# Performance work log

Measured on AMD Instinct MI355X. Metric: run time of the kernel, lower is better.

## Reference

```python
import jax, jax.numpy as jnp
import numpy as np

N = 50000
E = 800000
NODE_DIM = 15
HID = 64
HEADS = 4
NEG_SLOPE = 0.2


def _add_self_loops(edge_index, n):
    loops = jnp.arange(n, dtype=edge_index.dtype)
    src = jnp.concatenate([edge_index[0], loops])
    dst = jnp.concatenate([edge_index[1], loops])
    return src, dst


def gat_conv(x, edge_index, W, att_src, att_dst, bias, concat):
    # x: [N, F_in]; W: [F_in, heads*out]; att_*: [heads, out]; bias: [heads*out] or [out]
    n = x.shape[0]
    heads, out_dim = att_src.shape
    src, dst = _add_self_loops(edge_index, n)
    h = (x @ W).reshape(n, heads, out_dim)              # [N, H, D]
    a_src = jnp.sum(h * att_src[None], axis=-1)          # [N, H]
    a_dst = jnp.sum(h * att_dst[None], axis=-1)          # [N, H]
    e = a_src[src] + a_dst[dst]                          # [E', H]
    e = jnp.where(e > 0, e, NEG_SLOPE * e)               # LeakyReLU(0.2)
    # segment softmax over incoming edges of each dst node
    m = jax.ops.segment_max(e, dst, num_segments=n)      # [N, H]
    m = jnp.where(jnp.isfinite(m), m, 0.0)
    w = jnp.exp(e - m[dst])                              # [E', H]
    z = jax.ops.segment_sum(w, dst, num_segments=n)      # [N, H]
    alpha = w / z[dst]                                   # [E', H]
    msg = alpha[:, :, None] * h[src]                     # [E', H, D]
    out = jax.ops.segment_sum(msg, dst, num_segments=n)  # [N, H, D]
    if concat:
        return out.reshape(n, heads * out_dim) + bias
    return out.mean(axis=1) + bias


def setup_inputs() -> dict:
    key = jax.random.key(0)
    ks = jax.random.split(key, 11)
    x = jax.random.normal(ks[0], (N, NODE_DIM), dtype=jnp.float32)
    edge_index = jax.random.randint(ks[1], (2, E), 0, N, dtype=jnp.int64)
    s1 = 1.0 / np.sqrt(NODE_DIM)
    s2 = 1.0 / np.sqrt(HEADS * HID)
    return {
        "x": x,
        "edge_index": edge_index,
        "W1": jax.random.normal(ks[2], (NODE_DIM, HEADS * HID), dtype=jnp.float32) * s1,
        "att_src1": jax.random.normal(ks[3], (HEADS, HID), dtype=jnp.float32) * s2,
        "att_dst1": jax.random.normal(ks[4], (HEADS, HID), dtype=jnp.float32) * s2,
        "b1": jnp.zeros((HEADS * HID,), dtype=jnp.float32),
        "W2": jax.random.normal(ks[5], (HEADS * HID, HID), dtype=jnp.float32) * s2,
        "att_src2": jax.random.normal(ks[6], (1, HID), dtype=jnp.float32) * s2,
        "att_dst2": jax.random.normal(ks[7], (1, HID), dtype=jnp.float32) * s2,
        "b2": jnp.zeros((HID,), dtype=jnp.float32),
    }


def reference(x, edge_index, W1, att_src1, att_dst1, b1, W2, att_src2, att_dst2, b2):
    h = gat_conv(x, edge_index, W1, att_src1, att_dst1, b1, concat=True)   # [N, 256]
    h = jax.nn.elu(h)
    # dropout p=0.2 skipped (eval mode)
    h = gat_conv(h, edge_index, W2, att_src2, att_dst2, b2, concat=True)   # heads=1 -> [N, 64]
    return h.mean(axis=0)                                                   # [64]
```

## Files before the change

### kernel.cpp

```cpp
#include <hip/hip_runtime.h>
#include <hip/hip_fp16.h>

#define NNODES 50000
#define NEDGES 800000
#define NEG_SLOPE 0.2f
#define NTOT (NEDGES + NNODES)
#define NB_NODE ((NNODES + 255) / 256)
#define CHUNK 4096
#define NCHUNK ((NEDGES + CHUNK - 1) / CHUNK)
#define CAPB 4800
#define CNTSTRIDE 16

typedef _Float16 half8 __attribute__((ext_vector_type(8)));
typedef _Float16 half4 __attribute__((ext_vector_type(4)));
typedef float f32x4 __attribute__((ext_vector_type(4)));

__global__ void setup_kernel(const float* __restrict__ x, const float* __restrict__ W1,
                             const float* __restrict__ att_src, const float* __restrict__ att_dst,
                             const float* __restrict__ W2,
                             int* __restrict__ bucket_cnt, float* __restrict__ x16,
                             float* __restrict__ asrc4, float* __restrict__ adst4,
                             _Float16* __restrict__ W2T) {
    int b = blockIdx.x, t = threadIdx.x;
    __shared__ float swa[16][4], swd[16][4];
    if (t < 128) {
        int k = (t & 63) >> 2, h = t & 3;
        float s = 0.f;
        if (k < 15) {
            const float* att = (t < 64) ? att_src : att_dst;
#pragma unroll 16
            for (int d = 0; d < 64; ++d)
                s += W1[k * 256 + h * 64 + d] * att[h * 64 + d];
        }
        if (t < 64) swa[k][h] = s; else swd[k][h] = s;
    }
    int tid = b * 256 + t;
    if (tid < NB_NODE * CNTSTRIDE) bucket_cnt[tid] = 0;
    if (tid < 64 * 256) {
        int n = tid >> 8, k = tid & 255;
        W2T[n * 256 + k] = (_Float16)W2[k * 64 + n];
    }
    __syncthreads();
    int nid = tid;
    if (nid < NNODES) {
        float xv[16];
#pragma unroll
        for (int k = 0; k < 15; ++k) xv[k] = x[nid * 15 + k];
        xv[15] = 0.f;
#pragma unroll
        for (int k = 0; k < 16; k += 4)
            *(float4*)(x16 + (size_t)nid * 16 + k) = make_float4(xv[k], xv[k+1], xv[k+2], xv[k+3]);
        float ps[4] = {0.f, 0.f, 0.f, 0.f}, pd[4] = {0.f, 0.f, 0.f, 0.f};
#pragma unroll
        for (int k = 0; k < 15; ++k)
#pragma unroll
            for (int h = 0; h < 4; ++h) {
                ps[h] += xv[k] * swa[k][h];
                pd[h] += xv[k] * swd[k][h];
            }
        *(float4*)(asrc4 + nid * 4) = make_float4(ps[0], ps[1], ps[2], ps[3]);
        *(float4*)(adst4 + nid * 4) = make_float4(pd[0], pd[1], pd[2], pd[3]);
    }
}

__global__ void bucket_scatter(const int* __restrict__ srcs, const int* __restrict__ dsts,
                               int* __restrict__ bucket_cnt, int* __restrict__ bucketbuf) {
    int b = blockIdx.x, t = threadIdx.x;
    __shared__ unsigned short meta[CHUNK];
    __shared__ int lcnt[NB_NODE], lbase[NB_NODE];
    for (int i = t; i < NB_NODE; i += 256) lcnt[i] = 0;
    __syncthreads();
    int e0 = b * CHUNK;
    int e1 = e0 + CHUNK; if (e1 > NEDGES) e1 = NEDGES;
    for (int e = e0 + t; e < e1; e += 256) {
        int d = dsts[e];
        meta[e - e0] = (unsigned short)d;
        atomicAdd(&lcnt[d >> 8], 1);
    }
    __syncthreads();
    for (int i = t; i < NB_NODE; i += 256) {
        int c = lcnt[i];
        lbase[i] = c ? atomicAdd(&bucket_cnt[i * CNTSTRIDE], c) : 0;
    }
    __syncthreads();
    for (int i = t; i < NB_NODE; i += 256) lcnt[i] = 0;
    __syncthreads();
    for (int e = e0 + t; e < e1; e += 256) {
        int dv = meta[e - e0];
        int bk = dv >> 8;
        int pos = lbase[bk] + atomicAdd(&lcnt[bk], 1);
        if (pos < CAPB) bucketbuf[bk * CAPB + pos] = ((dv & 255) << 16) | srcs[e];
    }
}

__global__ void scanA(const int* __restrict__ bucket_cnt, const int* __restrict__ bucketbuf,
                      int* __restrict__ rowstart, int* __restrict__ partials) {
    int b = blockIdx.x, t = threadIdx.x, lane = t & 63, wid = t >> 6;
    __shared__ int hist[256];
    __shared__ int ws[4];
    int i = b * 256 + t;
    hist[t] = (i < NNODES) ? 1 : 0;
    __syncthreads();
    int n = bucket_cnt[b * CNTSTRIDE]; if (n > CAPB) n = CAPB;
    const int* buf = bucketbuf + (size_t)b * CAPB;
    for (int j = t; j < n; j += 256)
        atomicAdd(&hist[buf[j] >> 16], 1);
    __syncthreads();
    int v = (i < NNODES) ? hist[t] : 0;
    int incl = v;
#pragma unroll
    for (int off = 1; off < 64; off <<= 1) {
        int u = __shfl_up(incl, off, 64);
        if (lane >= off) incl += u;
    }
    if (lane == 63) ws[wid] = incl;
    __syncthreads();
    int w0 = ws[0], w1 = ws[1], w2 = ws[2], w3 = ws[3];
    int woff = (wid > 0 ? w0 : 0) + (wid > 1 ? w1 : 0) + (wid > 2 ? w2 : 0);
    if (i < NNODES) rowstart[i] = woff + (incl - v);
    if (t == 0) partials[b] = w0 + w1 + w2 + w3;
}

__global__ void scanB(const int* __restrict__ partials, int* __restrict__ blockoff,
                      int* __restrict__ rowstart, int nb) {
    int t = threadIdx.x, lane = t & 63, wid = t >> 6;
    int v = (t < nb) ? partials[t] : 0;
    int incl = v;
#pragma unroll
    for (int off = 1; off < 64; off <<= 1) {
        int u = __shfl_up(incl, off, 64);
        if (lane >= off) incl += u;
    }
    __shared__ int ws[4];
    if (lane == 63) ws[wid] = incl;
    __syncthreads();
    int w0 = ws[0], w1 = ws[1], w2 = ws[2], w3 = ws[3];
    int woff = (wid > 0 ? w0 : 0) + (wid > 1 ? w1 : 0) + (wid > 2 ? w2 : 0);
    if (t < nb) blockoff[t] = woff + (incl - v);
    if (t == 0) rowstart[NNODES] = w0 + w1 + w2 + w3;
}

__global__ void scanC(int* __restrict__ rowstart, const int* __restrict__ blockoff) {
    int b = blockIdx.x, t = threadIdx.x;
    int i = b * 256 + t;
    if (i < NNODES) rowstart[i] += blockoff[b];
}

__global__ void local_sort(const int* __restrict__ bucket_cnt, const int* __restrict__ bucketbuf,
                           const int* __restrict__ rowstart, int* __restrict__ srclist) {
    int b = blockIdx.x, t = threadIdx.x;
    __shared__ int cur[256];
    __shared__ int local[8192];
    int idx = b * 256 + t; if (idx > NNODES) idx = NNODES;
    int base = rowstart[b * 256];
    cur[t] = rowstart[idx] - base;
    __syncthreads();
    int nid = b * 256 + t;
    if (nid < NNODES) {
        int pos = atomicAdd(&cur[t], 1);
        local[pos] = nid;
    }
    int n = bucket_cnt[b * CNTSTRIDE]; if (n > CAPB) n = CAPB;
    const int* buf = bucketbuf + (size_t)b * CAPB;
    for (int i = t; i < n; i += 256) {
        int entry = buf[i];
        int pos = atomicAdd(&cur[entry >> 16], 1);
        local[pos] = entry & 0xFFFF;
    }
    __syncthreads();
    int endidx = (b + 1) * 256; if (endidx > NNODES) endidx = NNODES;
    int total = rowstart[endidx] - base;
    for (int i = t; i < total; i += 256) srclist[base + i] = local[i];
}

__global__ void layer1_aggr(const float* __restrict__ x16, const int* __restrict__ rowstart,
                            const int* __restrict__ srclist,
                            const float* __restrict__ asrc4, const float* __restrict__ adst4,
                            const float* __restrict__ W1, const float* __restrict__ b1,
                            __half* __restrict__ out1) {
    int wid = threadIdx.x >> 6, lane = threadIdx.x & 63;
    int nid = blockIdx.x * 4 + wid;
    int h = lane >> 4, k = lane & 15;
    int beg = __builtin_amdgcn_readfirstlane(rowstart[nid]);
    int end = __builtin_amdgcn_readfirstlane(rowstart[nid + 1]);
    float ad = adst4[nid * 4 + h];
    float acc = 0.f, zs = 0.f;
    int nfull = beg + ((end - beg) & ~3);
    for (int i0 = beg; i0 < nfull; i0 += 4) {
        int s0 = srclist[i0];
        int s1 = srclist[i0 + 1];
        int s2 = srclist[i0 + 2];
        int s3 = srclist[i0 + 3];
        float xv0 = x16[s0 * 16 + k];
        float xv1 = x16[s1 * 16 + k];
        float xv2 = x16[s2 * 16 + k];
        float xv3 = x16[s3 * 16 + k];
        float e0 = asrc4[s0 * 4 + h] + ad;
        float e1 = asrc4[s1 * 4 + h] + ad;
        float e2 = asrc4[s2 * 4 + h] + ad;
        float e3 = asrc4[s3 * 4 + h] + ad;
        e0 = fmaxf(e0, NEG_SLOPE * e0); e1 = fmaxf(e1, NEG_SLOPE * e1);
        e2 = fmaxf(e2, NEG_SLOPE * e2); e3 = fmaxf(e3, NEG_SLOPE * e3);
        float w0 = __expf(e0), w1 = __expf(e1), w2 = __expf(e2), w3 = __expf(e3);
        zs += w0 + w1 + w2 + w3;
        acc = fmaf(w0, xv0, acc);
        acc = fmaf(w1, xv1, acc);
        acc = fmaf(w2, xv2, acc);
        acc = fmaf(w3, xv3, acc);
    }
    for (int i = nfull; i < end; ++i) {
        int s = srclist[i];
        float xv = x16[s * 16 + k];
        float e = asrc4[s * 4 + h] + ad;
        e = fmaxf(e, NEG_SLOPE * e);
        float w = __expf(e);
        zs += w;
        acc = fmaf(w, xv, acc);
    }
    __shared__ float sacc[4][64];
    sacc[wid][lane] = acc * (1.f / zs);
    int c = lane, h2 = c >> 4;
    float o0 = 0.f, o1 = 0.f, o2 = 0.f, o3 = 0.f;
#pragma unroll
    for (int kk = 0; kk < 15; ++kk) {
        float a = sacc[wid][h2 * 16 + kk];
        float4 wv = *(const float4*)(W1 + kk * 256 + c * 4);
        o0 = fmaf(a, wv.x, o0); o1 = fmaf(a, wv.y, o1);
        o2 = fmaf(a, wv.z, o2); o3 = fmaf(a, wv.w, o3);
    }
    float4 bo = *(const float4*)(b1 + c * 4);
    o0 += bo.x; o1 += bo.y; o2 += bo.z; o3 += bo.w;
    o0 = o0 > 0.f ? o0 : __expf(o0) - 1.f;
    o1 = o1 > 0.f ? o1 : __expf(o1) - 1.f;
    o2 = o2 > 0.f ? o2 : __expf(o2) - 1.f;
    o3 = o3 > 0.f ? o3 : __expf(o3) - 1.f;
    half4 st;
    st[0] = (_Float16)o0; st[1] = (_Float16)o1; st[2] = (_Float16)o2; st[3] = (_Float16)o3;
    *(half4*)((_Float16*)out1 + (size_t)nid * 256 + c * 4) = st;
}


__global__ __launch_bounds__(256) void layer2_gemm(const __half* __restrict__ out1,
                                                   const _Float16* __restrict__ W2T,
                                                   __half* __restrict__ h2,
                                                   const float* __restrict__ att_src2,
                                                   const float* __restrict__ att_dst2,
                                                   float* __restrict__ as2,
                                                   float* __restrict__ ad2) {
    int w = threadIdx.x >> 6, lane = threadIdx.x & 63;
    int m16 = lane & 15, quad = lane >> 4;
    int r0 = blockIdx.x * 64 + w * 16;
    const _Float16* A = (const _Float16*)out1;
    f32x4 acc[4] = {{0.f,0.f,0.f,0.f},{0.f,0.f,0.f,0.f},{0.f,0.f,0.f,0.f},{0.f,0.f,0.f,0.f}};
    int row = r0 + m16; if (row >= NNODES) row = NNODES - 1;
#pragma unroll
    for (int k0 = 0; k0 < 256; k0 += 32) {
        half8 a = *(const half8*)(A + (size_t)row * 256 + k0 + quad * 8);
#pragma unroll
        for (int nt = 0; nt < 4; ++nt) {
            half8 b = *(const half8*)(W2T + (size_t)(nt * 16 + m16) * 256 + k0 + quad * 8);
            acc[nt] = __builtin_amdgcn_mfma_f32_16x16x32_f16(a, b, acc[nt], 0, 0, 0);
        }
    }
    __shared__ _Float16 tile[64][72];
#pragma unroll
    for (int nt = 0; nt < 4; ++nt)
#pragma unroll
        for (int r = 0; r < 4; ++r)
            tile[w * 16 + quad * 4 + r][nt * 16 + m16] = (_Float16)acc[nt][r];
    __syncthreads();
    int t = threadIdx.x;
    int trow = t >> 2, seg = t & 3;
    int rg = blockIdx.x * 64 + trow;
    if (rg < NNODES) {
        float4 v0 = *(float4*)&tile[trow][seg * 16];
        float4 v1 = *(float4*)&tile[trow][seg * 16 + 8];
        _Float16* dst = (_Float16*)h2 + (size_t)rg * 64 + seg * 16;
        *(float4*)dst = v0;
        *(float4*)(dst + 8) = v1;
        const _Float16* hv = &tile[trow][seg * 16];
        float ps = 0.f, pd = 0.f;
#pragma unroll
        for (int j = 0; j < 16; ++j) {
            float v = (float)hv[j];
            ps += v * att_src2[seg * 16 + j];
            pd += v * att_dst2[seg * 16 + j];
        }
        ps += __shfl_xor(ps, 1, 64); ps += __shfl_xor(ps, 2, 64);
        pd += __shfl_xor(pd, 1, 64); pd += __shfl_xor(pd, 2, 64);
        if (seg == 0) { as2[rg] = ps; ad2[rg] = pd; }
    }
}

__global__ void layer2_aggr(const __half* __restrict__ h2, const int* __restrict__ rowstart,
                            const int* __restrict__ srclist,
                            const float* __restrict__ as2, const float* __restrict__ ad2,
                            const float* __restrict__ b2, float* __restrict__ out2) {
    int wid = threadIdx.x >> 6, lane = threadIdx.x & 63;
    int nid = blockIdx.x * 4 + wid;
    int q = lane >> 4, c = lane & 15;
    int beg = __builtin_amdgcn_readfirstlane(rowstart[nid]);
    int end = __builtin_amdgcn_readfirstlane(rowstart[nid + 1]);
    float ad = ad2[nid];
    const __half* hb = h2 + c * 4;
    __half2 z16 = __float2half2_rn(0.f);
    __half2 acc0 = z16, acc1 = z16;
    float zs = 0.f;
    for (int i0 = beg; i0 < end; i0 += 16) {
#pragma unroll
        for (int u = 0; u < 4; ++u) {
            int i = i0 + q + 4 * u;
            bool valid = i < end;
            int s = valid ? srclist[i] : 0;
            float2 gv = *(const float2*)(hb + (size_t)s * 64);
            float e = as2[s] + ad;
            e = fmaxf(e, NEG_SLOPE * e);
            float w = valid ? __expf(e) : 0.f;
            zs += w;
            __half2 wh = __float2half2_rn(w);
            acc0 = __hfma2(wh, *(__half2*)&gv.x, acc0);
            acc1 = __hfma2(wh, *(__half2*)&gv.y, acc1);
        }
    }
    float2 f0 = __half22float2(acc0), f1 = __half22float2(acc1);
    float ax = f0.x, ay = f0.y, az = f1.x, aw = f1.y;
#pragma unroll
    for (int off = 16; off < 64; off <<= 1) {
        ax += __shfl_xor(ax, off, 64);
        ay += __shfl_xor(ay, off, 64);
        az += __shfl_xor(az, off, 64);
        aw += __shfl_xor(aw, off, 64);
        zs += __shfl_xor(zs, off, 64);
    }
    if (lane < 16) {
        float rz = 1.f / zs;
        float4 bo = ((const float4*)b2)[c];
        float4 st = make_float4(ax * rz + bo.x, ay * rz + bo.y,
                                az * rz + bo.z, aw * rz + bo.w);
        *(float4*)(out2 + (size_t)nid * 64 + c * 4) = st;
    }
}


__global__ void reduce_kernel(const float* __restrict__ out2, float* __restrict__ dout) {
    int t = threadIdx.x;
    int col = t & 63, sub = t >> 6;
    float acc = 0.f;
    for (int r = blockIdx.x * 4 + sub; r < NNODES; r += 256 * 4)
        acc += out2[r * 64 + col];
    __shared__ float sh[256];
    sh[t] = acc;
    __syncthreads();
    if (t < 64) {
        float v = sh[t] + sh[t + 64] + sh[t + 128] + sh[t + 192];
        atomicAdd(&dout[t], v * (1.0f / NNODES));
    }
}


extern "C" void kernel_launch(void* const* d_in, const int* in_sizes, int n_in,
                              void* d_out, int out_size, void* d_ws, size_t ws_size,
                              hipStream_t stream) {
    const float* x        = (const float*)d_in[0];
    const int*   ei       = (const int*)d_in[1];
    const float* W1       = (const float*)d_in[2];
    const float* att_src1 = (const float*)d_in[3];
    const float* att_dst1 = (const float*)d_in[4];
    const float* b1       = (const float*)d_in[5];
    const float* W2       = (const float*)d_in[6];
    const float* att_src2 = (const float*)d_in[7];
    const float* att_dst2 = (const float*)d_in[8];
    const float* b2       = (const float*)d_in[9];
    float* out = (float*)d_out;

    char* ws = (char*)d_ws;
    size_t off = 0;
    auto take = [&](size_t bytes) -> char* {
        char* p = ws + off;
        off = (off + bytes + 255) & ~(size_t)255;
        return p;
    };
    int*      bucket_cnt = (int*)take((size_t)NB_NODE * CNTSTRIDE * sizeof(int));
    int*      bucketbuf  = (int*)take((size_t)NB_NODE * CAPB * sizeof(int));
    int*      rowstart   = (int*)take((NNODES + 1) * sizeof(int));
    int*      partials   = (int*)take(256 * sizeof(int));
    int*      blockoff   = (int*)take(256 * sizeof(int));
    int*      srclist    = (int*)take(((size_t)NTOT + 16) * sizeof(int));
    float*    x16        = (float*)take((size_t)NNODES * 16 * sizeof(float));
    float*    asrc4      = (float*)take((size_t)NNODES * 4 * sizeof(float));
    float*    adst4      = (float*)take((size_t)NNODES * 4 * sizeof(float));
    __half*   out1       = (__half*)take((size_t)NNODES * 256 * sizeof(__half));
    _Float16* W2T        = (_Float16*)take(64 * 256 * sizeof(_Float16));
    __half*   h2         = (__half*)take((size_t)NNODES * 64 * sizeof(__half));
    float*    as2        = (float*)take((size_t)NNODES * sizeof(float));
    float*    ad2        = (float*)take((size_t)NNODES * sizeof(float));
    float*    out2       = (float*)take((size_t)NNODES * 64 * sizeof(float));

    const int* srcs = ei;
    const int* dsts = ei + NEDGES;

    hipMemsetAsync(d_out, 0, 64 * sizeof(float), stream);

    setup_kernel<<<NB_NODE, 256, 0, stream>>>(x, W1, att_src1, att_dst1, W2,
                                              bucket_cnt, x16, asrc4, adst4, W2T);
    bucket_scatter<<<NCHUNK, 256, 0, stream>>>(srcs, dsts, bucket_cnt, bucketbuf);
    scanA<<<NB_NODE, 256, 0, stream>>>(bucket_cnt, bucketbuf, rowstart, partials);
    scanB<<<1, 256, 0, stream>>>(partials, blockoff, rowstart, NB_NODE);
    scanC<<<NB_NODE, 256, 0, stream>>>(rowstart, blockoff);
    local_sort<<<NB_NODE, 256, 0, stream>>>(bucket_cnt, bucketbuf, rowstart, srclist);

    layer1_aggr<<<NNODES / 4, 256, 0, stream>>>(x16, rowstart, srclist, asrc4, adst4,
                                                W1, b1, out1);

    layer2_gemm<<<(NNODES + 63) / 64, 256, 0, stream>>>(out1, W2T, h2, att_src2, att_dst2,
                                                        as2, ad2);
    layer2_aggr<<<NNODES / 4, 256, 0, stream>>>(h2, rowstart, srclist, as2, ad2, b2, out2);

    reduce_kernel<<<256, 256, 0, stream>>>(out2, out);
}
```

Measured before the change: 223.1 us.

## Fuse setup with bucket scatter and precompute layer-1 edge weights in sort

Result: slower. 228.6 us (+2.4%).

```diff
diff --git a/kernel.cpp b/kernel.cpp
--- a/kernel.cpp
+++ b/kernel.cpp
@@ -15,81 +15,82 @@
 typedef _Float16 half4 __attribute__((ext_vector_type(4)));
 typedef float f32x4 __attribute__((ext_vector_type(4)));
 
-__global__ void setup_kernel(const float* __restrict__ x, const float* __restrict__ W1,
-                             const float* __restrict__ att_src, const float* __restrict__ att_dst,
-                             const float* __restrict__ W2,
-                             int* __restrict__ bucket_cnt, float* __restrict__ x16,
-                             float* __restrict__ asrc4, float* __restrict__ adst4,
-                             _Float16* __restrict__ W2T) {
-    int b = blockIdx.x, t = threadIdx.x;
-    __shared__ float swa[16][4], swd[16][4];
-    if (t < 128) {
-        int k = (t & 63) >> 2, h = t & 3;
-        float s = 0.f;
-        if (k < 15) {
-            const float* att = (t < 64) ? att_src : att_dst;
-#pragma unroll 16
-            for (int d = 0; d < 64; ++d)
-                s += W1[k * 256 + h * 64 + d] * att[h * 64 + d];
-        }
-        if (t < 64) swa[k][h] = s; else swd[k][h] = s;
-    }
-    int tid = b * 256 + t;
-    if (tid < NB_NODE * CNTSTRIDE) bucket_cnt[tid] = 0;
-    if (tid < 64 * 256) {
-        int n = tid >> 8, k = tid & 255;
-        W2T[n * 256 + k] = (_Float16)W2[k * 64 + n];
-    }
-    __syncthreads();
-    int nid = tid;
-    if (nid < NNODES) {
-        float xv[16];
-#pragma unroll
-        for (int k = 0; k < 15; ++k) xv[k] = x[nid * 15 + k];
-        xv[15] = 0.f;
-#pragma unroll
-        for (int k = 0; k < 16; k += 4)
-            *(float4*)(x16 + (size_t)nid * 16 + k) = make_float4(xv[k], xv[k+1], xv[k+2], xv[k+3]);
-        float ps[4] = {0.f, 0.f, 0.f, 0.f}, pd[4] = {0.f, 0.f, 0.f, 0.f};
-#pragma unroll
-        for (int k = 0; k < 15; ++k)
-#pragma unroll
-            for (int h = 0; h < 4; ++h) {
-                ps[h] += xv[k] * swa[k][h];
-                pd[h] += xv[k] * swd[k][h];
-            }
-        *(float4*)(asrc4 + nid * 4) = make_float4(ps[0], ps[1], ps[2], ps[3]);
-        *(float4*)(adst4 + nid * 4) = make_float4(pd[0], pd[1], pd[2], pd[3]);
-    }
-}
-
-__global__ void bucket_scatter(const int* __restrict__ srcs, const int* __restrict__ dsts,
-                               int* __restrict__ bucket_cnt, int* __restrict__ bucketbuf) {
-    int b = blockIdx.x, t = threadIdx.x;
+__global__ void setup_scatter(const float* __restrict__ x, const float* __restrict__ W1,
+                              const float* __restrict__ att_src, const float* __restrict__ att_dst,
+                              const float* __restrict__ W2,
+                              const int* __restrict__ srcs, const int* __restrict__ dsts,
+                              int* __restrict__ bucket_cnt, int* __restrict__ bucketbuf,
+                              float* __restrict__ x16, float* __restrict__ asrc4,
+                              float* __restrict__ adst4, _Float16* __restrict__ W2T) {
+    int t = threadIdx.x;
     __shared__ unsigned short meta[CHUNK];
     __shared__ int lcnt[NB_NODE], lbase[NB_NODE];
-    for (int i = t; i < NB_NODE; i += 256) lcnt[i] = 0;
-    __syncthreads();
-    int e0 = b * CHUNK;
-    int e1 = e0 + CHUNK; if (e1 > NEDGES) e1 = NEDGES;
-    for (int e = e0 + t; e < e1; e += 256) {
-        int d = dsts[e];
-        meta[e - e0] = (unsigned short)d;
-        atomicAdd(&lcnt[d >> 8], 1);
-    }
-    __syncthreads();
-    for (int i = t; i < NB_NODE; i += 256) {
-        int c = lcnt[i];
-        lbase[i] = c ? atomicAdd(&bucket_cnt[i * CNTSTRIDE], c) : 0;
-    }
-    __syncthreads();
-    for (int i = t; i < NB_NODE; i += 256) lcnt[i] = 0;
-    __syncthreads();
-    for (int e = e0 + t; e < e1; e += 256) {
-        int dv = meta[e - e0];
-        int bk = dv >> 8;
-        int pos = lbase[bk] + atomicAdd(&lcnt[bk], 1);
-        if (pos < CAPB) bucketbuf[bk * CAPB + pos] = ((dv & 255) << 16) | srcs[e];
+    __shared__ float swa[16][4], swd[16][4];
+    if (blockIdx.x < NCHUNK) {
+        int b = blockIdx.x;
+        for (int i = t; i < NB_NODE; i += 256) lcnt[i] = 0;
+        __syncthreads();
+        int e0 = b * CHUNK;
+        int e1 = e0 + CHUNK; if (e1 > NEDGES) e1 = NEDGES;
+        for (int e = e0 + t; e < e1; e += 256) {
+            int d = dsts[e];
+            meta[e - e0] = (unsigned short)d;
+            atomicAdd(&lcnt[d >> 8], 1);
+        }
+        __syncthreads();
+        for (int i = t; i < NB_NODE; i += 256) {
+            int c = lcnt[i];
+            lbase[i] = c ? atomicAdd(&bucket_cnt[i * CNTSTRIDE], c) : 0;
+        }
+        __syncthreads();
+        for (int i = t; i < NB_NODE; i += 256) lcnt[i] = 0;
+        __syncthreads();
+        for (int e = e0 + t; e < e1; e += 256) {
+            int dv = meta[e - e0];
+            int bk = dv >> 8;
+            int pos = lbase[bk] + atomicAdd(&lcnt[bk], 1);
+            if (pos < CAPB) bucketbuf[bk * CAPB + pos] = ((dv & 255) << 16) | srcs[e];
+        }
+    } else {
+        int b = blockIdx.x - NCHUNK;
+        if (t < 128) {
+            int k = (t & 63) >> 2, h = t & 3;
+            float s = 0.f;
+            if (k < 15) {
+                const float* att = (t < 64) ? att_src : att_dst;
+#pragma unroll 16
+                for (int d = 0; d < 64; ++d)
+                    s += W1[k * 256 + h * 64 + d] * att[h * 64 + d];
+            }
+            if (t < 64) swa[k][h] = s; else swd[k][h] = s;
+        }
+        int tid = b * 256 + t;
+        if (tid < 64 * 256) {
+            int n = tid >> 8, k = tid & 255;
+            W2T[n * 256 + k] = (_Float16)W2[k * 64 + n];
+        }
+        __syncthreads();
+        int nid = tid;
+        if (nid < NNODES) {
+            float xv[16];
+#pragma unroll
+            for (int k = 0; k < 15; ++k) xv[k] = x[nid * 15 + k];
+            xv[15] = 0.f;
+#pragma unroll
+            for (int k = 0; k < 16; k += 4)
+                *(float4*)(x16 + (size_t)nid * 16 + k) =
+                    make_float4(xv[k], xv[k+1], xv[k+2], xv[k+3]);
+            float ps[4] = {0.f, 0.f, 0.f, 0.f}, pd[4] = {0.f, 0.f, 0.f, 0.f};
+#pragma unroll
+            for (int k = 0; k < 15; ++k)
+#pragma unroll
+                for (int h = 0; h < 4; ++h) {
+                    ps[h] += xv[k] * swa[k][h];
+                    pd[h] += xv[k] * swd[k][h];
+                }
+            *(float4*)(asrc4 + nid * 4) = make_float4(ps[0], ps[1], ps[2], ps[3]);
+            *(float4*)(adst4 + nid * 4) = make_float4(pd[0], pd[1], pd[2], pd[3]);
+        }
     }
 }
 
@@ -147,35 +148,48 @@
 }
 
 __global__ void local_sort(const int* __restrict__ bucket_cnt, const int* __restrict__ bucketbuf,
-                           const int* __restrict__ rowstart, int* __restrict__ srclist) {
+                           const int* __restrict__ rowstart,
+                           const float4* __restrict__ asrc4, const float4* __restrict__ adst4,
+                           int* __restrict__ srclist, float4* __restrict__ sw4) {
     int b = blockIdx.x, t = threadIdx.x;
     __shared__ int cur[256];
     __shared__ int local[8192];
+    __shared__ float4 sadst[256];
     int idx = b * 256 + t; if (idx > NNODES) idx = NNODES;
     int base = rowstart[b * 256];
     cur[t] = rowstart[idx] - base;
-    __syncthreads();
     int nid = b * 256 + t;
+    if (nid < NNODES) sadst[t] = adst4[nid];
+    __syncthreads();
     if (nid < NNODES) {
         int pos = atomicAdd(&cur[t], 1);
-        local[pos] = nid;
+        local[pos] = (t << 16) | nid;
     }
     int n = bucket_cnt[b * CNTSTRIDE]; if (n > CAPB) n = CAPB;
     const int* buf = bucketbuf + (size_t)b * CAPB;
     for (int i = t; i < n; i += 256) {
         int entry = buf[i];
         int pos = atomicAdd(&cur[entry >> 16], 1);
-        local[pos] = entry & 0xFFFF;
+        local[pos] = entry;
     }
     __syncthreads();
     int endidx = (b + 1) * 256; if (endidx > NNODES) endidx = NNODES;
     int total = rowstart[endidx] - base;
-    for (int i = t; i < total; i += 256) srclist[base + i] = local[i];
+    for (int i = t; i < total; i += 256) {
+        int e = local[i];
+        int s = e & 0xFFFF, dl = e >> 16;
+        srclist[base + i] = s;
+        float4 as = asrc4[s];
+        float4 ad = sadst[dl];
+        float e0 = as.x + ad.x, e1 = as.y + ad.y, e2 = as.z + ad.z, e3 = as.w + ad.w;
+        e0 = fmaxf(e0, NEG_SLOPE * e0); e1 = fmaxf(e1, NEG_SLOPE * e1);
+        e2 = fmaxf(e2, NEG_SLOPE * e2); e3 = fmaxf(e3, NEG_SLOPE * e3);
+        sw4[base + i] = make_float4(__expf(e0), __expf(e1), __expf(e2), __expf(e3));
+    }
 }
 
 __global__ void layer1_aggr(const float* __restrict__ x16, const int* __restrict__ rowstart,
-                            const int* __restrict__ srclist,
-                            const float* __restrict__ asrc4, const float* __restrict__ adst4,
+                            const int* __restrict__ srclist, const float* __restrict__ sw4,
                             const float* __restrict__ W1, const float* __restrict__ b1,
                             __half* __restrict__ out1) {
     int wid = threadIdx.x >> 6, lane = threadIdx.x & 63;
@@ -183,39 +197,33 @@
     int h = lane >> 4, k = lane & 15;
     int beg = __builtin_amdgcn_readfirstlane(rowstart[nid]);
     int end = __builtin_amdgcn_readfirstlane(rowstart[nid + 1]);
-    float ad = adst4[nid * 4 + h];
     float acc = 0.f, zs = 0.f;
+    int i0 = beg;
     int nfull = beg + ((end - beg) & ~3);
-    for (int i0 = beg; i0 < nfull; i0 += 4) {
-        int s0 = srclist[i0];
-        int s1 = srclist[i0 + 1];
-        int s2 = srclist[i0 + 2];
-        int s3 = srclist[i0 + 3];
+    for (; i0 < nfull; i0 += 4) {
+        int s0 = __builtin_amdgcn_readfirstlane(srclist[i0]);
+        int s1 = __builtin_amdgcn_readfirstlane(srclist[i0 + 1]);
+        int s2 = __builtin_amdgcn_readfirstlane(srclist[i0 + 2]);
+        int s3 = __builtin_amdgcn_readfirstlane(srclist[i0 + 3]);
+        float w0 = sw4[(i0 + 0) * 4 + h];
+        float w1 = sw4[(i0 + 1) * 4 + h];
+        float w2 = sw4[(i0 + 2) * 4 + h];
+        float w3 = sw4[(i0 + 3) * 4 + h];
         float xv0 = x16[s0 * 16 + k];
         float xv1 = x16[s1 * 16 + k];
         float xv2 = x16[s2 * 16 + k];
         float xv3 = x16[s3 * 16 + k];
-        float e0 = asrc4[s0 * 4 + h] + ad;
-        float e1 = asrc4[s1 * 4 + h] + ad;
-        float e2 = asrc4[s2 * 4 + h] + ad;
-        float e3 = asrc4[s3 * 4 + h] + ad;
-        e0 = fmaxf(e0, NEG_SLOPE * e0); e1 = fmaxf(e1, NEG_SLOPE * e1);
-        e2 = fmaxf(e2, NEG_SLOPE * e2); e3 = fmaxf(e3, NEG_SLOPE * e3);
-        float w0 = __expf(e0), w1 = __expf(e1), w2 = __expf(e2), w3 = __expf(e3);
-        zs += w0 + w1 + w2 + w3;
+        zs += (w0 + w1) + (w2 + w3);
         acc = fmaf(w0, xv0, acc);
         acc = fmaf(w1, xv1, acc);
         acc = fmaf(w2, xv2, acc);
         acc = fmaf(w3, xv3, acc);
     }
-    for (int i = nfull; i < end; ++i) {
-        int s = srclist[i];
-        float xv = x16[s * 16 + k];
-        float e = asrc4[s * 4 + h] + ad;
-        e = fmaxf(e, NEG_SLOPE * e);
-        float w = __expf(e);
+    for (; i0 < end; ++i0) {
+        int s = __builtin_amdgcn_readfirstlane(srclist[i0]);
+        float w = sw4[i0 * 4 + h];
         zs += w;
-        acc = fmaf(w, xv, acc);
+        acc = fmaf(w, x16[s * 16 + k], acc);
     }
     __shared__ float sacc[4][64];
     sacc[wid][lane] = acc * (1.f / zs);
@@ -386,6 +394,7 @@
     int*      partials   = (int*)take(256 * sizeof(int));
     int*      blockoff   = (int*)take(256 * sizeof(int));
     int*      srclist    = (int*)take(((size_t)NTOT + 16) * sizeof(int));
+    float*    sw4        = (float*)take(((size_t)NTOT + 16) * 4 * sizeof(float));
     float*    x16        = (float*)take((size_t)NNODES * 16 * sizeof(float));
     float*    asrc4      = (float*)take((size_t)NNODES * 4 * sizeof(float));
     float*    adst4      = (float*)take((size_t)NNODES * 4 * sizeof(float));
@@ -400,17 +409,19 @@
     const int* dsts = ei + NEDGES;
 
     hipMemsetAsync(d_out, 0, 64 * sizeof(float), stream);
-
-    setup_kernel<<<NB_NODE, 256, 0, stream>>>(x, W1, att_src1, att_dst1, W2,
-                                              bucket_cnt, x16, asrc4, adst4, W2T);
-    bucket_scatter<<<NCHUNK, 256, 0, stream>>>(srcs, dsts, bucket_cnt, bucketbuf);
+    hipMemsetAsync(bucket_cnt, 0, (size_t)NB_NODE * CNTSTRIDE * sizeof(int), stream);
+
+    setup_scatter<<<NCHUNK + NB_NODE, 256, 0, stream>>>(x, W1, att_src1, att_dst1, W2,
+                                                        srcs, dsts, bucket_cnt, bucketbuf,
+                                                        x16, asrc4, adst4, W2T);
     scanA<<<NB_NODE, 256, 0, stream>>>(bucket_cnt, bucketbuf, rowstart, partials);
     scanB<<<1, 256, 0, stream>>>(partials, blockoff, rowstart, NB_NODE);
     scanC<<<NB_NODE, 256, 0, stream>>>(rowstart, blockoff);
-    local_sort<<<NB_NODE, 256, 0, stream>>>(bucket_cnt, bucketbuf, rowstart, srclist);
-
-    layer1_aggr<<<NNODES / 4, 256, 0, stream>>>(x16, rowstart, srclist, asrc4, adst4,
-                                                W1, b1, out1);
+    local_sort<<<NB_NODE, 256, 0, stream>>>(bucket_cnt, bucketbuf, rowstart,
+                                            (const float4*)asrc4, (const float4*)adst4,
+                                            srclist, (float4*)sw4);
+
+    layer1_aggr<<<NNODES / 4, 256, 0, stream>>>(x16, rowstart, srclist, sw4, W1, b1, out1);
 
     layer2_gemm<<<(NNODES + 63) / 64, 256, 0, stream>>>(out1, W2T, h2, att_src2, att_dst2,
                                                         as2, ad2);
```
